# Performance work log

Measured on AMD Instinct MI355X. Metric: run time of the kernel, lower is better.

The kernel has to match this reference:

```python
import jax, jax.numpy as jnp
import numpy as np

# Config (from TheoreticalConfig, scaled to production size)
B = 4096          # batch_size
S = 128           # seq_len (max_seq_len)
DIM_Q = 512
DIM_Z = 64
DIM_U = 512
HID_V = 512       # assumed net_V hidden width
T_OFF = 20        # T_offline
T_ON = 10         # T_online
DT = 0.1
STIFF = 0.1       # stiffness
CSTIFF = 0.1      # contact_stiffness
MIN_DIM = min(DIM_U, DIM_Q)  # == DIM_Q here


def setup_inputs() -> dict:
    key = jax.random.key(0)
    ks = jax.random.split(key, 10)
    f32 = jnp.float32
    return {
        "u_seq": jax.random.normal(ks[0], (B, S, DIM_U), f32),
        "q0_off": jax.random.normal(ks[1], (B, DIM_Q), f32) * 0.1,
        "p0_off": jax.random.normal(ks[2], (B, DIM_Q), f32) * 0.1,
        "q0_on": jax.random.normal(ks[3], (B, DIM_Q), f32) * 0.1,
        "p0_on": jax.random.normal(ks[4], (B, DIM_Q), f32) * 0.1,
        "z": jax.random.normal(ks[5], (1, DIM_Z), f32) * 0.1,
        "W1": jax.random.normal(ks[6], (DIM_Q + DIM_Z, HID_V), f32) / np.sqrt(DIM_Q + DIM_Z).astype(np.float32),
        "b1": jnp.zeros((HID_V,), f32),
        "W2": jax.random.normal(ks[7], (HID_V, 1), f32) / np.sqrt(HID_V).astype(np.float32),
        "b2": jnp.zeros((1,), f32),
    }


def _net_V(qz, W1, b1, W2, b2):
    # small MLP potential: [B, dim_q+dim_z] -> [B, 1]
    return jnp.tanh(qz @ W1 + b1) @ W2 + b2


def _compute_H(q, p, s, z, W1, b1, W2, b2):
    # H^c = K + V_quad + V_net + Phi, all [B, 1]
    K = 0.5 * jnp.sum(p * p, axis=-1, keepdims=True)
    V_quad = 0.5 * STIFF * jnp.sum(q * q, axis=-1, keepdims=True)
    V_net = _net_V(jnp.concatenate([q, z], axis=-1), W1, b1, W2, b2)
    Phi = 0.5 * CSTIFF * s * s
    return K + V_quad + V_net + Phi


def reference(u_seq, q0_off, p0_off, q0_on, p0_on, z, W1, b1, W2, b2):
    zb = jnp.broadcast_to(z, (B, DIM_Z))
    s = jnp.zeros((B, 1), u_seq.dtype)

    # ---- evolve_offline: symplectic-ish leapfrog with friction, T_OFF-1 steps ----
    F0_off = _compute_H(q0_off, p0_off, s, zb, W1, b1, W2, b2)

    def off_step(carry, _):
        q, p = carry
        q_new = q + DT * p                     # q += dt * grad_p (grad_p = p)
        p_new = (p - DT * (STIFF * q)) * 0.99  # p -= dt * grad_q (grad_q = stiff*q_old), then damping
        return (q_new, p_new), None

    (qf, pf), _ = jax.lax.scan(off_step, (q0_off, p0_off), None, length=T_OFF - 1)
    Ff_off = _compute_H(qf, pf, s, zb, W1, b1, W2, b2)
    offline_F = jnp.concatenate([F0_off, Ff_off], axis=1)  # [B, 2]

    # ---- evolve_online: port-coupled integration for min(S, T_ON) steps ----
    F0_on = _compute_H(q0_on, p0_on, s, zb, W1, b1, W2, b2)
    steps = min(S, T_ON)

    def on_step(carry, u_t):
        q, p = carry
        # p_new[:, :MIN_DIM] = p - dt*stiff*q + dt*0.1*u_t ; MIN_DIM == DIM_Q so full update
        p_new = (p - DT * (STIFF * q) + DT * (0.1 * u_t)) * 0.99
        q_new = q + DT * p_new
        return (q_new, p_new), None

    u_scan = jnp.transpose(u_seq[:, :steps, :MIN_DIM], (1, 0, 2))  # [steps, B, dim_q]
    (qf2, pf2), _ = jax.lax.scan(on_step, (q0_on, p0_on), u_scan)
    Ff_on = _compute_H(qf2, pf2, s, zb, W1, b1, W2, b2)
    online_F = jnp.concatenate([F0_on, Ff_on], axis=1)  # [B, 2]

    q_trajectory = qf2[:, None, :]  # [B, 1, dim_q]
    return offline_F, online_F, q_trajectory
```

## Files before the change

### kernel.cpp

```cpp
#include <hip/hip_runtime.h>
#include <hip/hip_bf16.h>

#define BB 4096
#define SS 128
#define DIMQ 512
#define DIMZ 64
#define HIDV 512

typedef __attribute__((ext_vector_type(8))) short sh8;
typedef __attribute__((ext_vector_type(4))) float f32x4;
typedef __attribute__((ext_vector_type(4))) unsigned short us4;

__device__ inline unsigned short f2bf(float f) {
    unsigned u = __float_as_uint(f);
    return (unsigned short)((u + 0x7fffu + ((u >> 16) & 1u)) >> 16);
}

__global__ __launch_bounds__(256) void k_states_prep(
        const float* __restrict__ u, const float* __restrict__ q0off,
        const float* __restrict__ p0off, const float* __restrict__ q0on,
        const float* __restrict__ p0on, const float* __restrict__ b2,
        const float* __restrict__ W1, const float* __restrict__ z,
        const float* __restrict__ b1,
        unsigned short* __restrict__ Qall, unsigned short* __restrict__ W1qT,
        float* __restrict__ cvec, float* __restrict__ out,
        float* __restrict__ qtraj,
        float R00, float R01, float R10, float R11) {
    if (blockIdx.x >= 2048) {
        int pbi = blockIdx.x - 2048;
        __shared__ float tile[32][33];
        int bx = pbi & 15, by = pbi >> 4;
        int k0 = by * 32, n0 = bx * 32;
        int tx = threadIdx.x & 31, tg = threadIdx.x >> 5;
        #pragma unroll
        for (int rr = 0; rr < 4; rr++) {
            int ty = tg * 4 + rr;
            tile[ty][tx] = W1[(size_t)(k0 + ty) * HIDV + n0 + tx];
        }
        __syncthreads();
        #pragma unroll
        for (int rr = 0; rr < 4; rr++) {
            int ty = tg * 4 + rr;
            W1qT[(size_t)(n0 + ty) * DIMQ + k0 + tx] = f2bf(tile[tx][ty]);
        }
        if (pbi < 2) {
            int h = pbi * 256 + threadIdx.x;
            float acc = b1[h];
            #pragma unroll 8
            for (int k = 0; k < DIMZ; k++) acc += z[k] * W1[(size_t)(DIMQ + k) * HIDV + h];
            cvec[h] = acc;
        }
        return;
    }
    int t = threadIdx.x;
    int half = t >> 7;
    int tc = t & 127;
    int b = blockIdx.x * 2 + half;
    int j = tc * 4;
    size_t idx = (size_t)b * DIMQ + j;
    float q[4], p[4], qo[4], po[4];
    *(float4*)q  = *(const float4*)(q0off + idx);
    *(float4*)p  = *(const float4*)(p0off + idx);
    *(float4*)qo = *(const float4*)(q0on + idx);
    *(float4*)po = *(const float4*)(p0on + idx);

    float sums[8] = {0, 0, 0, 0, 0, 0, 0, 0};
    us4 w0, w1, w2, w3;
    float q2[4], p2[4];
    #pragma unroll
    for (int c = 0; c < 4; c++) {
        float qq = q[c], pp = p[c];
        sums[0] += qq * qq;
        sums[1] += pp * pp;
        float qf = R00 * qq + R01 * pp;
        float pf = R10 * qq + R11 * pp;
        sums[2] += qf * qf;
        sums[3] += pf * pf;
        w0[c] = f2bf(qq);
        w1[c] = f2bf(qf);
        q2[c] = qo[c]; p2[c] = po[c];
        sums[4] += q2[c] * q2[c];
        sums[5] += p2[c] * p2[c];
        w2[c] = f2bf(q2[c]);
    }
    *(us4*)(Qall + idx) = w0;
    *(us4*)(Qall + (size_t)(BB + b) * DIMQ + j) = w1;
    *(us4*)(Qall + (size_t)(2 * BB + b) * DIMQ + j) = w2;

    const float* ub = u + (size_t)b * SS * DIMQ + j;
    #pragma unroll
    for (int st = 0; st < 10; st++) {
        float uv[4];
        *(float4*)uv = *(const float4*)(ub + (size_t)st * DIMQ);
        #pragma unroll
        for (int c = 0; c < 4; c++) {
            p2[c] = (p2[c] - 0.1f * (0.1f * q2[c]) + 0.1f * (0.1f * uv[c])) * 0.99f;
            q2[c] = q2[c] + 0.1f * p2[c];
        }
    }
    #pragma unroll
    for (int c = 0; c < 4; c++) {
        sums[6] += q2[c] * q2[c];
        sums[7] += p2[c] * p2[c];
        w3[c] = f2bf(q2[c]);
    }
    *(us4*)(Qall + (size_t)(3 * BB + b) * DIMQ + j) = w3;
    *(float4*)(qtraj + idx) = *(float4*)q2;

    __shared__ float red[2][2][8];
    int lane = t & 63, wv = (t >> 6) & 1;
    #pragma unroll
    for (int k = 0; k < 8; k++) {
        float v = sums[k];
        #pragma unroll
        for (int m = 1; m < 64; m <<= 1) v += __shfl_xor(v, m, 64);
        if (lane == 0) red[half][wv][k] = v;
    }
    __syncthreads();
    if (tc < 4) {
        int e = tc;
        float sq = red[half][0][2 * e] + red[half][1][2 * e];
        float sp = red[half][0][2 * e + 1] + red[half][1][2 * e + 1];
        float F = 0.5f * sp + 0.05f * sq + b2[0];
        size_t o = (size_t)b * 2 + (e & 1) + (size_t)(e >> 1) * 2 * BB;
        out[o] = F;
    }
}

__global__ __launch_bounds__(256) void k_gemm(
        const unsigned short* __restrict__ Qall, const unsigned short* __restrict__ W1qT,
        const float* __restrict__ cvec, const float* __restrict__ W2,
        float* __restrict__ out) {
    __shared__ __attribute__((aligned(16))) char lds[65536];
    const int t = threadIdx.x;
    const int lane = t & 63;
    const int w = t >> 6;
    const int wr = w >> 1, wc = w & 1;
    const int rowBase = blockIdx.x * 128;
    const int colBase = blockIdx.y * 128;

    f32x4 acc[4][4] = {};

    auto STAGE = [&](int kt, int buf) {
        char* ldsA = lds + buf * 32768;
        char* ldsB = ldsA + 16384;
        #pragma unroll
        for (int i = 0; i < 4; i++) {
            unsigned chunk = i * 256 + t;
            unsigned r = chunk >> 3;
            unsigned scb = (chunk & 7) ^ (r & 7);
            const unsigned short* srcA = Qall + (size_t)(rowBase + r) * 512 + (unsigned)kt * 64 + scb * 8;
            __builtin_amdgcn_global_load_lds(
                (const __attribute__((address_space(1))) unsigned int*)(const void*)srcA,
                (__attribute__((address_space(3))) unsigned int*)(void*)(ldsA + chunk * 16), 16, 0, 0);
            const unsigned short* srcB = W1qT + (size_t)(colBase + r) * 512 + (unsigned)kt * 64 + scb * 8;
            __builtin_amdgcn_global_load_lds(
                (const __attribute__((address_space(1))) unsigned int*)(const void*)srcB,
                (__attribute__((address_space(3))) unsigned int*)(void*)(ldsB + chunk * 16), 16, 0, 0);
        }
    };

    STAGE(0, 0);
    asm volatile("s_waitcnt vmcnt(0)" ::: "memory");
    __builtin_amdgcn_s_barrier();

    for (int kt = 0; kt < 8; kt++) {
        int cur = kt & 1;
        if (kt < 7) STAGE(kt + 1, cur ^ 1);
        char* ldsA = lds + cur * 32768;
        char* ldsB = ldsA + 16384;
        #pragma unroll
        for (int ks = 0; ks < 2; ks++) {
            sh8 af[4], bf_[4];
            int kb = ks * 64 + ((lane >> 4) << 4);
            #pragma unroll
            for (int mi = 0; mi < 4; mi++) {
                int m = wr * 64 + mi * 16 + (lane & 15);
                af[mi] = *(const sh8*)(ldsA + m * 128 + (kb ^ ((m & 7) << 4)));
            }
            #pragma unroll
            for (int ni = 0; ni < 4; ni++) {
                int n = wc * 64 + ni * 16 + (lane & 15);
                bf_[ni] = *(const sh8*)(ldsB + n * 128 + (kb ^ ((n & 7) << 4)));
            }
            #pragma unroll
            for (int mi = 0; mi < 4; mi++)
                #pragma unroll
                for (int ni = 0; ni < 4; ni++)
                    acc[mi][ni] = __builtin_amdgcn_mfma_f32_16x16x32_bf16(af[mi], bf_[ni], acc[mi][ni], 0, 0, 0);
        }
        asm volatile("s_waitcnt vmcnt(0) lgkmcnt(0)" ::: "memory");
        __builtin_amdgcn_s_barrier();
    }

    float w2v[4], cv[4];
    #pragma unroll
    for (int ni = 0; ni < 4; ni++) {
        int n = colBase + wc * 64 + ni * 16 + (lane & 15);
        w2v[ni] = W2[n];
        cv[ni] = cvec[n];
    }
    #pragma unroll
    for (int mi = 0; mi < 4; mi++) {
        #pragma unroll
        for (int r = 0; r < 4; r++) {
            float partial = 0.f;
            #pragma unroll
            for (int ni = 0; ni < 4; ni++)
                partial += tanhf(acc[mi][ni][r] + cv[ni]) * w2v[ni];
            partial += __shfl_xor(partial, 1, 64);
            partial += __shfl_xor(partial, 2, 64);
            partial += __shfl_xor(partial, 4, 64);
            partial += __shfl_xor(partial, 8, 64);
            if ((lane & 15) == 0) {
                int row = rowBase + wr * 64 + mi * 16 + ((lane >> 4) << 2) + r;
                int e = row >> 12, bb = row & 4095;
                size_t o = (size_t)bb * 2 + (e & 1) + (size_t)(e >> 1) * 2 * BB;
                atomicAdd(out + o, partial);
            }
        }
    }
}

extern "C" void kernel_launch(void* const* d_in, const int* in_sizes, int n_in,
                              void* d_out, int out_size, void* d_ws, size_t ws_size,
                              hipStream_t stream) {
    const float* u     = (const float*)d_in[0];
    const float* q0off = (const float*)d_in[1];
    const float* p0off = (const float*)d_in[2];
    const float* q0on  = (const float*)d_in[3];
    const float* p0on  = (const float*)d_in[4];
    const float* z     = (const float*)d_in[5];
    const float* W1    = (const float*)d_in[6];
    const float* b1    = (const float*)d_in[7];
    const float* W2    = (const float*)d_in[8];
    const float* b2    = (const float*)d_in[9];
    float* out = (float*)d_out;

    char* ws = (char*)d_ws;
    unsigned short* Qall = (unsigned short*)ws;
    unsigned short* W1qT = (unsigned short*)(ws + 16777216);
    float* cvec = (float*)(ws + 16777216 + 524288);

    double a00 = 1, a01 = 0, a10 = 0, a11 = 1;
    const double m00 = 1.0, m01 = 0.1, m10 = -0.1 * 0.1 * 0.99, m11 = 0.99;
    for (int i = 0; i < 19; i++) {
        double n00 = m00 * a00 + m01 * a10;
        double n01 = m00 * a01 + m01 * a11;
        double n10 = m10 * a00 + m11 * a10;
        double n11 = m10 * a01 + m11 * a11;
        a00 = n00; a01 = n01; a10 = n10; a11 = n11;
    }

    k_states_prep<<<2304, 256, 0, stream>>>(u, q0off, p0off, q0on, p0on, b2,
                                            W1, z, b1, Qall, W1qT, cvec, out,
                                            out + 4 * BB,
                                            (float)a00, (float)a01, (float)a10, (float)a11);
    k_gemm<<<dim3(128, 4), 256, 0, stream>>>(Qall, W1qT, cvec, W2, out);
}
```

Before: 43.26 us.

## Fuse bf16 conversion into GEMM A-loads and overlap GEMM with state integration

Removes the intermediate bf16 Qall buffer. The GEMM now reads the fp32 q states directly, applying the offline rotation and converting to bf16 on the fly into LDS. Three of the four GEMM row-groups run inside the same kernel as the online integration, so the two can overlap, while a tail kernel handles the final-state GEMM from qtraj and folds in the accumulated Vnet values. This trades the 16MB workspace round trip for three launches, register-staged A loads that need more VGPRs, and larger fp32 A reads.

Measured after the change: 67.79 us. 56.7% more time.

```diff
diff --git a/kernel.cpp b/kernel.cpp
--- a/kernel.cpp
+++ b/kernel.cpp
@@ -9,53 +9,183 @@
 
 typedef __attribute__((ext_vector_type(8))) short sh8;
 typedef __attribute__((ext_vector_type(4))) float f32x4;
-typedef __attribute__((ext_vector_type(4))) unsigned short us4;
 
 __device__ inline unsigned short f2bf(float f) {
     unsigned u = __float_as_uint(f);
     return (unsigned short)((u + 0x7fffu + ((u >> 16) & 1u)) >> 16);
 }
 
-__global__ __launch_bounds__(256) void k_states_prep(
+__global__ __launch_bounds__(256) void k_prep(const float* __restrict__ W1,
+        const float* __restrict__ z, const float* __restrict__ b1,
+        unsigned short* __restrict__ W1qT, float* __restrict__ cvec,
+        float* __restrict__ Vnet) {
+    __shared__ float tile[32][33];
+    int bx = blockIdx.x & 15, by = blockIdx.x >> 4;
+    int k0 = by * 32, n0 = bx * 32;
+    int tx = threadIdx.x & 31, tg = threadIdx.x >> 5;
+    #pragma unroll
+    for (int rr = 0; rr < 4; rr++) {
+        int ty = tg * 4 + rr;
+        tile[ty][tx] = W1[(size_t)(k0 + ty) * HIDV + n0 + tx];
+    }
+    __syncthreads();
+    #pragma unroll
+    for (int rr = 0; rr < 4; rr++) {
+        int ty = tg * 4 + rr;
+        W1qT[(size_t)(n0 + ty) * DIMQ + k0 + tx] = f2bf(tile[tx][ty]);
+    }
+    if (blockIdx.x < 2) {
+        int h = blockIdx.x * 256 + threadIdx.x;
+        float acc = b1[h];
+        #pragma unroll 8
+        for (int k = 0; k < DIMZ; k++) acc += z[k] * W1[(size_t)(DIMQ + k) * HIDV + h];
+        cvec[h] = acc;
+    }
+    if (blockIdx.x < 12) {
+        int i = blockIdx.x * 1024 + threadIdx.x * 4;
+        float4 zv = {0.f, 0.f, 0.f, 0.f};
+        *(float4*)(Vnet + i) = zv;
+    }
+}
+
+__global__ __launch_bounds__(256) void k_main(
         const float* __restrict__ u, const float* __restrict__ q0off,
         const float* __restrict__ p0off, const float* __restrict__ q0on,
         const float* __restrict__ p0on, const float* __restrict__ b2,
-        const float* __restrict__ W1, const float* __restrict__ z,
-        const float* __restrict__ b1,
-        unsigned short* __restrict__ Qall, unsigned short* __restrict__ W1qT,
-        float* __restrict__ cvec, float* __restrict__ out,
-        float* __restrict__ qtraj,
+        const unsigned short* __restrict__ W1qT, const float* __restrict__ cvec,
+        const float* __restrict__ W2, float* __restrict__ Vnet,
+        float* __restrict__ out, float* __restrict__ qtraj,
         float R00, float R01, float R10, float R11) {
-    if (blockIdx.x >= 2048) {
-        int pbi = blockIdx.x - 2048;
-        __shared__ float tile[32][33];
-        int bx = pbi & 15, by = pbi >> 4;
-        int k0 = by * 32, n0 = bx * 32;
-        int tx = threadIdx.x & 31, tg = threadIdx.x >> 5;
-        #pragma unroll
-        for (int rr = 0; rr < 4; rr++) {
-            int ty = tg * 4 + rr;
-            tile[ty][tx] = W1[(size_t)(k0 + ty) * HIDV + n0 + tx];
-        }
-        __syncthreads();
-        #pragma unroll
-        for (int rr = 0; rr < 4; rr++) {
-            int ty = tg * 4 + rr;
-            W1qT[(size_t)(n0 + ty) * DIMQ + k0 + tx] = f2bf(tile[tx][ty]);
-        }
-        if (pbi < 2) {
-            int h = pbi * 256 + threadIdx.x;
-            float acc = b1[h];
-            #pragma unroll 8
-            for (int k = 0; k < DIMZ; k++) acc += z[k] * W1[(size_t)(DIMQ + k) * HIDV + h];
-            cvec[h] = acc;
+    __shared__ __attribute__((aligned(16))) char lds[65536];
+    const int t = threadIdx.x;
+
+    if (blockIdx.x < 384) {
+        const int gi = blockIdx.x;
+        const int e = gi >> 7;
+        const int rtc = gi & 127;
+        const int rowBase = (rtc >> 2) * 128;
+        const int colBase = (rtc & 3) * 128;
+        const int lane = t & 63;
+        const int w = t >> 6;
+        const int wr = w >> 1, wc = w & 1;
+        const float* srcA = (e == 2) ? q0on : q0off;
+
+        f32x4 acc[4][4] = {};
+        float4 Aq[4][2], Ap[4][2];
+
+        auto LOAD_A = [&](int kt) {
+            #pragma unroll
+            for (int i = 0; i < 4; i++) {
+                int ch = i * 256 + t, r = ch >> 3, cb = ch & 7;
+                const float* ba = srcA + (size_t)(rowBase + r) * 512 + kt * 64 + cb * 8;
+                Aq[i][0] = *(const float4*)ba;
+                Aq[i][1] = *(const float4*)(ba + 4);
+                if (e == 1) {
+                    const float* bp = p0off + (size_t)(rowBase + r) * 512 + kt * 64 + cb * 8;
+                    Ap[i][0] = *(const float4*)bp;
+                    Ap[i][1] = *(const float4*)(bp + 4);
+                }
+            }
+        };
+        auto WRITE_A = [&](int buf) {
+            char* dA = lds + buf * 16384;
+            #pragma unroll
+            for (int i = 0; i < 4; i++) {
+                int ch = i * 256 + t, r = ch >> 3, cb = ch & 7;
+                sh8 v;
+                #pragma unroll
+                for (int c2 = 0; c2 < 8; c2++) {
+                    float qv = (c2 < 4) ? Aq[i][0][c2] : Aq[i][1][c2 - 4];
+                    if (e == 1) {
+                        float pv = (c2 < 4) ? Ap[i][0][c2] : Ap[i][1][c2 - 4];
+                        qv = R00 * qv + R01 * pv;
+                    }
+                    v[c2] = (short)f2bf(qv);
+                }
+                *(sh8*)(dA + r * 128 + ((cb << 4) ^ ((r & 7) << 4))) = v;
+            }
+        };
+        auto STAGE_B = [&](int kt, int buf) {
+            char* dB = lds + 32768 + buf * 16384;
+            #pragma unroll
+            for (int i = 0; i < 4; i++) {
+                unsigned ch = i * 256 + t;
+                unsigned r = ch >> 3;
+                unsigned scb = (ch & 7) ^ (r & 7);
+                const unsigned short* src = W1qT + (size_t)(colBase + r) * 512 + (unsigned)kt * 64 + scb * 8;
+                __builtin_amdgcn_global_load_lds(
+                    (const __attribute__((address_space(1))) unsigned int*)(const void*)src,
+                    (__attribute__((address_space(3))) unsigned int*)(void*)(dB + ch * 16), 16, 0, 0);
+            }
+        };
+
+        LOAD_A(0);
+        STAGE_B(0, 0);
+        WRITE_A(0);
+        asm volatile("s_waitcnt vmcnt(0) lgkmcnt(0)" ::: "memory");
+        __builtin_amdgcn_s_barrier();
+
+        for (int kt = 0; kt < 8; kt++) {
+            int cur = kt & 1;
+            if (kt < 7) { LOAD_A(kt + 1); STAGE_B(kt + 1, cur ^ 1); }
+            char* ldsA = lds + cur * 16384;
+            char* ldsB = lds + 32768 + cur * 16384;
+            #pragma unroll
+            for (int ks = 0; ks < 2; ks++) {
+                sh8 af[4], bf_[4];
+                int kb = ks * 64 + ((lane >> 4) << 4);
+                #pragma unroll
+                for (int mi = 0; mi < 4; mi++) {
+                    int m = wr * 64 + mi * 16 + (lane & 15);
+                    af[mi] = *(const sh8*)(ldsA + m * 128 + (kb ^ ((m & 7) << 4)));
+                }
+                #pragma unroll
+                for (int ni = 0; ni < 4; ni++) {
+                    int n = wc * 64 + ni * 16 + (lane & 15);
+                    bf_[ni] = *(const sh8*)(ldsB + n * 128 + (kb ^ ((n & 7) << 4)));
+                }
+                #pragma unroll
+                for (int mi = 0; mi < 4; mi++)
+                    #pragma unroll
+                    for (int ni = 0; ni < 4; ni++)
+                        acc[mi][ni] = __builtin_amdgcn_mfma_f32_16x16x32_bf16(af[mi], bf_[ni], acc[mi][ni], 0, 0, 0);
+            }
+            if (kt < 7) WRITE_A(cur ^ 1);
+            asm volatile("s_waitcnt vmcnt(0) lgkmcnt(0)" ::: "memory");
+            __builtin_amdgcn_s_barrier();
+        }
+
+        float w2v[4], cv[4];
+        #pragma unroll
+        for (int ni = 0; ni < 4; ni++) {
+            int n = colBase + wc * 64 + ni * 16 + (lane & 15);
+            w2v[ni] = W2[n];
+            cv[ni] = cvec[n];
+        }
+        #pragma unroll
+        for (int mi = 0; mi < 4; mi++) {
+            #pragma unroll
+            for (int r = 0; r < 4; r++) {
+                float partial = 0.f;
+                #pragma unroll
+                for (int ni = 0; ni < 4; ni++)
+                    partial += tanhf(acc[mi][ni][r] + cv[ni]) * w2v[ni];
+                partial += __shfl_xor(partial, 1, 64);
+                partial += __shfl_xor(partial, 2, 64);
+                partial += __shfl_xor(partial, 4, 64);
+                partial += __shfl_xor(partial, 8, 64);
+                if ((lane & 15) == 0) {
+                    int row = rowBase + wr * 64 + mi * 16 + ((lane >> 4) << 2) + r;
+                    atomicAdd(Vnet + e * BB + row, partial);
+                }
+            }
         }
         return;
     }
-    int t = threadIdx.x;
+
     int half = t >> 7;
     int tc = t & 127;
-    int b = blockIdx.x * 2 + half;
+    int b = (blockIdx.x - 384) * 2 + half;
     int j = tc * 4;
     size_t idx = (size_t)b * DIMQ + j;
     float q[4], p[4], qo[4], po[4];
@@ -65,7 +195,6 @@
     *(float4*)po = *(const float4*)(p0on + idx);
 
     float sums[8] = {0, 0, 0, 0, 0, 0, 0, 0};
-    us4 w0, w1, w2, w3;
     float q2[4], p2[4];
     #pragma unroll
     for (int c = 0; c < 4; c++) {
@@ -76,17 +205,10 @@
         float pf = R10 * qq + R11 * pp;
         sums[2] += qf * qf;
         sums[3] += pf * pf;
-        w0[c] = f2bf(qq);
-        w1[c] = f2bf(qf);
         q2[c] = qo[c]; p2[c] = po[c];
         sums[4] += q2[c] * q2[c];
         sums[5] += p2[c] * p2[c];
-        w2[c] = f2bf(q2[c]);
-    }
-    *(us4*)(Qall + idx) = w0;
-    *(us4*)(Qall + (size_t)(BB + b) * DIMQ + j) = w1;
-    *(us4*)(Qall + (size_t)(2 * BB + b) * DIMQ + j) = w2;
-
+    }
     const float* ub = u + (size_t)b * SS * DIMQ + j;
     #pragma unroll
     for (int st = 0; st < 10; st++) {
@@ -102,73 +224,102 @@
     for (int c = 0; c < 4; c++) {
         sums[6] += q2[c] * q2[c];
         sums[7] += p2[c] * p2[c];
-        w3[c] = f2bf(q2[c]);
-    }
-    *(us4*)(Qall + (size_t)(3 * BB + b) * DIMQ + j) = w3;
+    }
     *(float4*)(qtraj + idx) = *(float4*)q2;
 
-    __shared__ float red[2][2][8];
+    float* red = (float*)lds;
     int lane = t & 63, wv = (t >> 6) & 1;
     #pragma unroll
     for (int k = 0; k < 8; k++) {
         float v = sums[k];
         #pragma unroll
         for (int m = 1; m < 64; m <<= 1) v += __shfl_xor(v, m, 64);
-        if (lane == 0) red[half][wv][k] = v;
+        if (lane == 0) red[(half * 2 + wv) * 8 + k] = v;
     }
     __syncthreads();
     if (tc < 4) {
         int e = tc;
-        float sq = red[half][0][2 * e] + red[half][1][2 * e];
-        float sp = red[half][0][2 * e + 1] + red[half][1][2 * e + 1];
+        float sq = red[(half * 2) * 8 + 2 * e] + red[(half * 2 + 1) * 8 + 2 * e];
+        float sp = red[(half * 2) * 8 + 2 * e + 1] + red[(half * 2 + 1) * 8 + 2 * e + 1];
         float F = 0.5f * sp + 0.05f * sq + b2[0];
         size_t o = (size_t)b * 2 + (e & 1) + (size_t)(e >> 1) * 2 * BB;
         out[o] = F;
     }
 }
 
-__global__ __launch_bounds__(256) void k_gemm(
-        const unsigned short* __restrict__ Qall, const unsigned short* __restrict__ W1qT,
+__global__ __launch_bounds__(256) void k_tail(
+        const float* __restrict__ qtraj, const unsigned short* __restrict__ W1qT,
         const float* __restrict__ cvec, const float* __restrict__ W2,
-        float* __restrict__ out) {
+        const float* __restrict__ Vnet, float* __restrict__ out) {
     __shared__ __attribute__((aligned(16))) char lds[65536];
     const int t = threadIdx.x;
+
+    if (blockIdx.x >= 128) {
+        int i = (blockIdx.x - 128) * 256 + t;
+        int e = i >> 12, b = i & 4095;
+        size_t o = (size_t)b * 2 + (e & 1) + (size_t)(e >> 1) * 2 * BB;
+        out[o] += Vnet[i];
+        return;
+    }
+
+    const int gi = blockIdx.x;
+    const int rowBase = (gi >> 2) * 128;
+    const int colBase = (gi & 3) * 128;
     const int lane = t & 63;
     const int w = t >> 6;
     const int wr = w >> 1, wc = w & 1;
-    const int rowBase = blockIdx.x * 128;
-    const int colBase = blockIdx.y * 128;
 
     f32x4 acc[4][4] = {};
-
-    auto STAGE = [&](int kt, int buf) {
-        char* ldsA = lds + buf * 32768;
-        char* ldsB = ldsA + 16384;
+    float4 Aq[4][2];
+
+    auto LOAD_A = [&](int kt) {
         #pragma unroll
         for (int i = 0; i < 4; i++) {
-            unsigned chunk = i * 256 + t;
-            unsigned r = chunk >> 3;
-            unsigned scb = (chunk & 7) ^ (r & 7);
-            const unsigned short* srcA = Qall + (size_t)(rowBase + r) * 512 + (unsigned)kt * 64 + scb * 8;
+            int ch = i * 256 + t, r = ch >> 3, cb = ch & 7;
+            const float* ba = qtraj + (size_t)(rowBase + r) * 512 + kt * 64 + cb * 8;
+            Aq[i][0] = *(const float4*)ba;
+            Aq[i][1] = *(const float4*)(ba + 4);
+        }
+    };
+    auto WRITE_A = [&](int buf) {
+        char* dA = lds + buf * 16384;
+        #pragma unroll
+        for (int i = 0; i < 4; i++) {
+            int ch = i * 256 + t, r = ch >> 3, cb = ch & 7;
+            sh8 v;
+            #pragma unroll
+            for (int c2 = 0; c2 < 8; c2++) {
+                float qv = (c2 < 4) ? Aq[i][0][c2] : Aq[i][1][c2 - 4];
+                v[c2] = (short)f2bf(qv);
+            }
+            *(sh8*)(dA + r * 128 + ((cb << 4) ^ ((r & 7) << 4))) = v;
+        }
+    };
+    auto STAGE_B = [&](int kt, int buf) {
+        char* dB = lds + 32768 + buf * 16384;
+        #pragma unroll
+        for (int i = 0; i < 4; i++) {
+            unsigned ch = i * 256 + t;
+            unsigned r = ch >> 3;
+            unsigned scb = (ch & 7) ^ (r & 7);
+            const unsigned short* src = W1qT + (size_t)(colBase + r) * 512 + (unsigned)kt * 64 + scb * 8;
             __builtin_amdgcn_global_load_lds(
-                (const __attribute__((address_space(1))) unsigned int*)(const void*)srcA,
-                (__attribute__((address_space(3))) unsigned int*)(void*)(ldsA + chunk * 16), 16, 0, 0);
-            const unsigned short* srcB = W1qT + (size_t)(colBase + r) * 512 + (unsigned)kt * 64 + scb * 8;
-            __builtin_amdgcn_global_load_lds(
-                (const __attribute__((address_space(1))) unsigned int*)(const void*)srcB,
-                (__attribute__((address_space(3))) unsigned int*)(void*)(ldsB + chunk * 16), 16, 0, 0);
+                (const __attribute__((address_space(1))) unsigned int*)(const void*)src,
+                (__attribute__((address_space(3))) unsigned int*)(void*)(dB + ch * 16), 16, 0, 0);
         }
     };
 
-    STAGE(0, 0);
-    asm volatile("s_waitcnt vmcnt(0)" ::: "memory");
+    LOAD_A(0);
+    STAGE_B(0, 0);
+    WRITE_A(0);
+    asm volatile("s_waitcnt vmcnt(0) lgkmcnt(0)" ::: "memory");
     __builtin_amdgcn_s_barrier();
 
     for (int kt = 0; kt < 8; kt++) {
         int cur = kt & 1;
-        if (kt < 7) STAGE(kt + 1, cur ^ 1);
-        char* ldsA = lds + cur * 32768;
-        char* ldsB = ldsA + 16384;
+        if (kt < 7) { LOAD_A(kt + 1); STAGE_B(kt + 1, cur ^ 1); }
+        char* ldsA = lds + cur * 16384;
+        char* ldsB = lds + 32768 + cur * 16384;
         #pragma unroll
         for (int ks = 0; ks < 2; ks++) {
             sh8 af[4], bf_[4];
@@ -189,6 +340,7 @@
                 for (int ni = 0; ni < 4; ni++)
                     acc[mi][ni] = __builtin_amdgcn_mfma_f32_16x16x32_bf16(af[mi], bf_[ni], acc[mi][ni], 0, 0, 0);
         }
+        if (kt < 7) WRITE_A(cur ^ 1);
         asm volatile("s_waitcnt vmcnt(0) lgkmcnt(0)" ::: "memory");
         __builtin_amdgcn_s_barrier();
     }
@@ -213,10 +365,8 @@
             partial += __shfl_xor(partial, 4, 64);
             partial += __shfl_xor(partial, 8, 64);
             if ((lane & 15) == 0) {
-                int row = rowBase + wr * 64 + mi * 16 + ((lane >> 4) << 2) + r;
-                int e = row >> 12, bb = row & 4095;
-                size_t o = (size_t)bb * 2 + (e & 1) + (size_t)(e >> 1) * 2 * BB;
-                atomicAdd(out + o, partial);
+                int b = rowBase + wr * 64 + mi * 16 + ((lane >> 4) << 2) + r;
+                atomicAdd(out + 2 * BB + (size_t)b * 2 + 1, partial);
             }
         }
     }
@@ -236,11 +386,12 @@
     const float* W2    = (const float*)d_in[8];
     const float* b2    = (const float*)d_in[9];
     float* out = (float*)d_out;
+    float* qtraj = out + 4 * BB;
 
     char* ws = (char*)d_ws;
-    unsigned short* Qall = (unsigned short*)ws;
-    unsigned short* W1qT = (unsigned short*)(ws + 16777216);
-    float* cvec = (float*)(ws + 16777216 + 524288);
+    unsigned short* W1qT = (unsigned short*)ws;
+    float* cvec = (float*)(ws + 524288);
+    float* Vnet = (float*)(ws + 524288 + 2048);
 
     double a00 = 1, a01 = 0, a10 = 0, a11 = 1;
     const double m00 = 1.0, m01 = 0.1, m10 = -0.1 * 0.1 * 0.99, m11 = 0.99;
@@ -252,9 +403,9 @@
         a00 = n00; a01 = n01; a10 = n10; a11 = n11;
     }
 
-    k_states_prep<<<2304, 256, 0, stream>>>(u, q0off, p0off, q0on, p0on, b2,
-                                            W1, z, b1, Qall, W1qT, cvec, out,
-                                            out + 4 * BB,
-                                            (float)a00, (float)a01, (float)a10, (float)a11);
-    k_gemm<<<dim3(128, 4), 256, 0, stream>>>(Qall, W1qT, cvec, W2, out);
+    k_prep<<<256, 256, 0, stream>>>(W1, z, b1, W1qT, cvec, Vnet);
+    k_main<<<2432, 256, 0, stream>>>(u, q0off, p0off, q0on, p0on, b2,
+                                     W1qT, cvec, W2, Vnet, out, qtraj,
+                                     (float)a00, (float)a01, (float)a10, (float)a11);
+    k_tail<<<176, 256, 0, stream>>>(qtraj, W1qT, cvec, W2, Vnet, out);
 }
```

## Fuse GEMM for input states into the elementwise kernel, reading fp32 directly

Applied to the files above, without the earlier changes.

Drops the bf16 staging buffer Qall. The three GEMM slices that depend only on inputs (initial offline, propagated offline, initial online) now run as extra blocks interleaved inside the elementwise kernel. Those blocks load fp32 rows straight from global memory, apply the 2x2 propagation matrix and convert to bf16 in registers. The final-online slice runs in a tail kernel that reads qtraj and also adds the accumulated Vnet into the output. This removes the 16 MB bf16 write and re-read and overlaps GEMM with the u-streaming work, but the GEMM gives up LDS staging and double buffering and uses smaller 64x128 tiles. It also adds a third kernel launch.

New measurement: 140.0 us. 3.24x slower.

```diff
diff --git a/kernel.cpp b/kernel.cpp
--- a/kernel.cpp
+++ b/kernel.cpp
@@ -9,53 +9,143 @@
 
 typedef __attribute__((ext_vector_type(8))) short sh8;
 typedef __attribute__((ext_vector_type(4))) float f32x4;
-typedef __attribute__((ext_vector_type(4))) unsigned short us4;
 
 __device__ inline unsigned short f2bf(float f) {
     unsigned u = __float_as_uint(f);
     return (unsigned short)((u + 0x7fffu + ((u >> 16) & 1u)) >> 16);
 }
 
-__global__ __launch_bounds__(256) void k_states_prep(
+__device__ __forceinline__ void gemm_tile(
+        int gi, bool isE1, const float* __restrict__ A0, const float* __restrict__ A1,
+        float R00, float R01,
+        const unsigned short* __restrict__ W1qT, const float* __restrict__ cvec,
+        const float* __restrict__ W2, float* __restrict__ tgt, int tgtMode, int t) {
+    const int lane = t & 63;
+    const int w = t >> 6;
+    const int rowBase = (gi >> 2) * 64 + (w >> 1) * 32;
+    const int colBase = (gi & 3) * 128 + (w & 1) * 64;
+    const int rr = lane & 15, g = lane >> 4;
+
+    f32x4 acc[2][4] = {};
+    for (int kt = 0; kt < 16; kt++) {
+        sh8 af[2];
+        #pragma unroll
+        for (int mi = 0; mi < 2; mi++) {
+            const float* pa = A0 + (size_t)(rowBase + mi * 16 + rr) * 512 + kt * 32 + g * 8;
+            float4 x0 = *(const float4*)pa;
+            float4 x1 = *(const float4*)(pa + 4);
+            if (isE1) {
+                const float* pb = A1 + (size_t)(rowBase + mi * 16 + rr) * 512 + kt * 32 + g * 8;
+                float4 y0 = *(const float4*)pb;
+                float4 y1 = *(const float4*)(pb + 4);
+                #pragma unroll
+                for (int j = 0; j < 4; j++) {
+                    x0[j] = R00 * x0[j] + R01 * y0[j];
+                    x1[j] = R00 * x1[j] + R01 * y1[j];
+                }
+            }
+            sh8 v;
+            #pragma unroll
+            for (int j = 0; j < 4; j++) {
+                v[j] = (short)f2bf(x0[j]);
+                v[4 + j] = (short)f2bf(x1[j]);
+            }
+            af[mi] = v;
+        }
+        sh8 bf_[4];
+        #pragma unroll
+        for (int ni = 0; ni < 4; ni++)
+            bf_[ni] = *(const sh8*)(W1qT + (size_t)(colBase + ni * 16 + rr) * 512 + kt * 32 + g * 8);
+        #pragma unroll
+        for (int mi = 0; mi < 2; mi++)
+            #pragma unroll
+            for (int ni = 0; ni < 4; ni++)
+                acc[mi][ni] = __builtin_amdgcn_mfma_f32_16x16x32_bf16(af[mi], bf_[ni], acc[mi][ni], 0, 0, 0);
+    }
+    float w2v[4], cv[4];
+    #pragma unroll
+    for (int ni = 0; ni < 4; ni++) {
+        int n = colBase + ni * 16 + rr;
+        w2v[ni] = W2[n];
+        cv[ni] = cvec[n];
+    }
+    #pragma unroll
+    for (int mi = 0; mi < 2; mi++) {
+        #pragma unroll
+        for (int r = 0; r < 4; r++) {
+            float s = 0.f;
+            #pragma unroll
+            for (int ni = 0; ni < 4; ni++)
+                s += tanhf(acc[mi][ni][r] + cv[ni]) * w2v[ni];
+            s += __shfl_xor(s, 1, 64);
+            s += __shfl_xor(s, 2, 64);
+            s += __shfl_xor(s, 4, 64);
+            s += __shfl_xor(s, 8, 64);
+            if (rr == 0) {
+                int row = rowBase + mi * 16 + g * 4 + r;
+                if (tgtMode == 0) atomicAdd(tgt + row, s);
+                else atomicAdd(tgt + (size_t)row * 2, s);
+            }
+        }
+    }
+}
+
+__global__ __launch_bounds__(256) void k_prep(const float* __restrict__ W1,
+        const float* __restrict__ z, const float* __restrict__ b1,
+        unsigned short* __restrict__ W1qT, float* __restrict__ cvec,
+        float* __restrict__ Vnet) {
+    __shared__ float tile[32][33];
+    int bx = blockIdx.x & 15, by = blockIdx.x >> 4;
+    int k0 = by * 32, n0 = bx * 32;
+    int tx = threadIdx.x & 31, tg = threadIdx.x >> 5;
+    #pragma unroll
+    for (int rr = 0; rr < 4; rr++) {
+        int ty = tg * 4 + rr;
+        tile[ty][tx] = W1[(size_t)(k0 + ty) * HIDV + n0 + tx];
+    }
+    __syncthreads();
+    #pragma unroll
+    for (int rr = 0; rr < 4; rr++) {
+        int ty = tg * 4 + rr;
+        W1qT[(size_t)(n0 + ty) * DIMQ + k0 + tx] = f2bf(tile[tx][ty]);
+    }
+    if (blockIdx.x < 2) {
+        int h = blockIdx.x * 256 + threadIdx.x;
+        float acc = b1[h];
+        #pragma unroll 8
+        for (int k = 0; k < DIMZ; k++) acc += z[k] * W1[(size_t)(DIMQ + k) * HIDV + h];
+        cvec[h] = acc;
+    }
+    if (blockIdx.x < 12) {
+        int i = blockIdx.x * 1024 + threadIdx.x * 4;
+        float4 zv = {0.f, 0.f, 0.f, 0.f};
+        *(float4*)(Vnet + i) = zv;
+    }
+}
+
+__global__ __launch_bounds__(256, 4) void k_main(
         const float* __restrict__ u, const float* __restrict__ q0off,
         const float* __restrict__ p0off, const float* __restrict__ q0on,
         const float* __restrict__ p0on, const float* __restrict__ b2,
-        const float* __restrict__ W1, const float* __restrict__ z,
-        const float* __restrict__ b1,
-        unsigned short* __restrict__ Qall, unsigned short* __restrict__ W1qT,
-        float* __restrict__ cvec, float* __restrict__ out,
-        float* __restrict__ qtraj,
+        const unsigned short* __restrict__ W1qT, const float* __restrict__ cvec,
+        const float* __restrict__ W2, float* __restrict__ Vnet,
+        float* __restrict__ out, float* __restrict__ qtraj,
         float R00, float R01, float R10, float R11) {
-    if (blockIdx.x >= 2048) {
-        int pbi = blockIdx.x - 2048;
-        __shared__ float tile[32][33];
-        int bx = pbi & 15, by = pbi >> 4;
-        int k0 = by * 32, n0 = bx * 32;
-        int tx = threadIdx.x & 31, tg = threadIdx.x >> 5;
-        #pragma unroll
-        for (int rr = 0; rr < 4; rr++) {
-            int ty = tg * 4 + rr;
-            tile[ty][tx] = W1[(size_t)(k0 + ty) * HIDV + n0 + tx];
-        }
-        __syncthreads();
-        #pragma unroll
-        for (int rr = 0; rr < 4; rr++) {
-            int ty = tg * 4 + rr;
-            W1qT[(size_t)(n0 + ty) * DIMQ + k0 + tx] = f2bf(tile[tx][ty]);
-        }
-        if (pbi < 2) {
-            int h = pbi * 256 + threadIdx.x;
-            float acc = b1[h];
-            #pragma unroll 8
-            for (int k = 0; k < DIMZ; k++) acc += z[k] * W1[(size_t)(DIMQ + k) * HIDV + h];
-            cvec[h] = acc;
-        }
+    const int t = threadIdx.x;
+    const int bid = blockIdx.x;
+    const int g1 = (int)(((long)bid * 768) / 2816);
+    const int g2 = (int)(((long)(bid + 1) * 768) / 2816);
+    if (g2 > g1) {
+        int e = g1 >> 8, gi = g1 & 255;
+        gemm_tile(gi, e == 1, (e == 2) ? q0on : q0off, p0off, R00, R01,
+                  W1qT, cvec, W2, Vnet + e * BB, 0, t);
         return;
     }
-    int t = threadIdx.x;
+
+    int sb = bid - g1;
     int half = t >> 7;
     int tc = t & 127;
-    int b = blockIdx.x * 2 + half;
+    int b = sb * 2 + half;
     int j = tc * 4;
     size_t idx = (size_t)b * DIMQ + j;
     float q[4], p[4], qo[4], po[4];
@@ -65,7 +155,6 @@
     *(float4*)po = *(const float4*)(p0on + idx);
 
     float sums[8] = {0, 0, 0, 0, 0, 0, 0, 0};
-    us4 w0, w1, w2, w3;
     float q2[4], p2[4];
     #pragma unroll
     for (int c = 0; c < 4; c++) {
@@ -76,17 +165,10 @@
         float pf = R10 * qq + R11 * pp;
         sums[2] += qf * qf;
         sums[3] += pf * pf;
-        w0[c] = f2bf(qq);
-        w1[c] = f2bf(qf);
         q2[c] = qo[c]; p2[c] = po[c];
         sums[4] += q2[c] * q2[c];
         sums[5] += p2[c] * p2[c];
-        w2[c] = f2bf(q2[c]);
-    }
-    *(us4*)(Qall + idx) = w0;
-    *(us4*)(Qall + (size_t)(BB + b) * DIMQ + j) = w1;
-    *(us4*)(Qall + (size_t)(2 * BB + b) * DIMQ + j) = w2;
-
+    }
     const float* ub = u + (size_t)b * SS * DIMQ + j;
     #pragma unroll
     for (int st = 0; st < 10; st++) {
@@ -102,124 +184,43 @@
     for (int c = 0; c < 4; c++) {
         sums[6] += q2[c] * q2[c];
         sums[7] += p2[c] * p2[c];
-        w3[c] = f2bf(q2[c]);
-    }
-    *(us4*)(Qall + (size_t)(3 * BB + b) * DIMQ + j) = w3;
+    }
     *(float4*)(qtraj + idx) = *(float4*)q2;
 
-    __shared__ float red[2][2][8];
+    __shared__ float red[32];
     int lane = t & 63, wv = (t >> 6) & 1;
     #pragma unroll
     for (int k = 0; k < 8; k++) {
         float v = sums[k];
         #pragma unroll
         for (int m = 1; m < 64; m <<= 1) v += __shfl_xor(v, m, 64);
-        if (lane == 0) red[half][wv][k] = v;
+        if (lane == 0) red[(half * 2 + wv) * 8 + k] = v;
     }
     __syncthreads();
     if (tc < 4) {
         int e = tc;
-        float sq = red[half][0][2 * e] + red[half][1][2 * e];
-        float sp = red[half][0][2 * e + 1] + red[half][1][2 * e + 1];
+        float sq = red[(half * 2) * 8 + 2 * e] + red[(half * 2 + 1) * 8 + 2 * e];
+        float sp = red[(half * 2) * 8 + 2 * e + 1] + red[(half * 2 + 1) * 8 + 2 * e + 1];
         float F = 0.5f * sp + 0.05f * sq + b2[0];
         size_t o = (size_t)b * 2 + (e & 1) + (size_t)(e >> 1) * 2 * BB;
         out[o] = F;
     }
 }
 
-__global__ __launch_bounds__(256) void k_gemm(
-        const unsigned short* __restrict__ Qall, const unsigned short* __restrict__ W1qT,
+__global__ __launch_bounds__(256) void k_tail(
+        const float* __restrict__ qtraj, const unsigned short* __restrict__ W1qT,
         const float* __restrict__ cvec, const float* __restrict__ W2,
-        float* __restrict__ out) {
-    __shared__ __attribute__((aligned(16))) char lds[65536];
+        const float* __restrict__ Vnet, float* __restrict__ out) {
     const int t = threadIdx.x;
-    const int lane = t & 63;
-    const int w = t >> 6;
-    const int wr = w >> 1, wc = w & 1;
-    const int rowBase = blockIdx.x * 128;
-    const int colBase = blockIdx.y * 128;
-
-    f32x4 acc[4][4] = {};
-
-    auto STAGE = [&](int kt, int buf) {
-        char* ldsA = lds + buf * 32768;
-        char* ldsB = ldsA + 16384;
-        #pragma unroll
-        for (int i = 0; i < 4; i++) {
-            unsigned chunk = i * 256 + t;
-            unsigned r = chunk >> 3;
-            unsigned scb = (chunk & 7) ^ (r & 7);
-            const unsigned short* srcA = Qall + (size_t)(rowBase + r) * 512 + (unsigned)kt * 64 + scb * 8;
-            __builtin_amdgcn_global_load_lds(
-                (const __attribute__((address_space(1))) unsigned int*)(const void*)srcA,
-                (__attribute__((address_space(3))) unsigned int*)(void*)(ldsA + chunk * 16), 16, 0, 0);
-            const unsigned short* srcB = W1qT + (size_t)(colBase + r) * 512 + (unsigned)kt * 64 + scb * 8;
-            __builtin_amdgcn_global_load_lds(
-                (const __attribute__((address_space(1))) unsigned int*)(const void*)srcB,
-                (__attribute__((address_space(3))) unsigned int*)(void*)(ldsB + chunk * 16), 16, 0, 0);
-        }
-    };
-
-    STAGE(0, 0);
-    asm volatile("s_waitcnt vmcnt(0)" ::: "memory");
-    __builtin_amdgcn_s_barrier();
-
-    for (int kt = 0; kt < 8; kt++) {
-        int cur = kt & 1;
-        if (kt < 7) STAGE(kt + 1, cur ^ 1);
-        char* ldsA = lds + cur * 32768;
-        char* ldsB = ldsA + 16384;
-        #pragma unroll
-        for (int ks = 0; ks < 2; ks++) {
-            sh8 af[4], bf_[4];
-            int kb = ks * 64 + ((lane >> 4) << 4);
-            #pragma unroll
-            for (int mi = 0; mi < 4; mi++) {
-                int m = wr * 64 + mi * 16 + (lane & 15);
-                af[mi] = *(const sh8*)(ldsA + m * 128 + (kb ^ ((m & 7) << 4)));
-            }
-            #pragma unroll
-            for (int ni = 0; ni < 4; ni++) {
-                int n = wc * 64 + ni * 16 + (lane & 15);
-                bf_[ni] = *(const sh8*)(ldsB + n * 128 + (kb ^ ((n & 7) << 4)));
-            }
-            #pragma unroll
-            for (int mi = 0; mi < 4; mi++)
-                #pragma unroll
-                for (int ni = 0; ni < 4; ni++)
-                    acc[mi][ni] = __builtin_amdgcn_mfma_f32_16x16x32_bf16(af[mi], bf_[ni], acc[mi][ni], 0, 0, 0);
-        }
-        asm volatile("s_waitcnt vmcnt(0) lgkmcnt(0)" ::: "memory");
-        __builtin_amdgcn_s_barrier();
-    }
-
-    float w2v[4], cv[4];
-    #pragma unroll
-    for (int ni = 0; ni < 4; ni++) {
-        int n = colBase + wc * 64 + ni * 16 + (lane & 15);
-        w2v[ni] = W2[n];
-        cv[ni] = cvec[n];
-    }
-    #pragma unroll
-    for (int mi = 0; mi < 4; mi++) {
-        #pragma unroll
-        for (int r = 0; r < 4; r++) {
-            float partial = 0.f;
-            #pragma unroll
-            for (int ni = 0; ni < 4; ni++)
-                partial += tanhf(acc[mi][ni][r] + cv[ni]) * w2v[ni];
-            partial += __shfl_xor(partial, 1, 64);
-            partial += __shfl_xor(partial, 2, 64);
-            partial += __shfl_xor(partial, 4, 64);
-            partial += __shfl_xor(partial, 8, 64);
-            if ((lane & 15) == 0) {
-                int row = rowBase + wr * 64 + mi * 16 + ((lane >> 4) << 2) + r;
-                int e = row >> 12, bb = row & 4095;
-                size_t o = (size_t)bb * 2 + (e & 1) + (size_t)(e >> 1) * 2 * BB;
-                atomicAdd(out + o, partial);
-            }
-        }
-    }
+    if (blockIdx.x >= 256) {
+        int i = (blockIdx.x - 256) * 256 + t;
+        int e = i >> 12, b = i & 4095;
+        size_t o = (size_t)b * 2 + (e & 1) + (size_t)(e >> 1) * 2 * BB;
+        out[o] += Vnet[i];
+        return;
+    }
+    gemm_tile(blockIdx.x, false, qtraj, nullptr, 0.f, 0.f,
+              W1qT, cvec, W2, out + 2 * BB + 1, 1, t);
 }
 
 extern "C" void kernel_launch(void* const* d_in, const int* in_sizes, int n_in,
@@ -236,11 +237,12 @@
     const float* W2    = (const float*)d_in[8];
     const float* b2    = (const float*)d_in[9];
     float* out = (float*)d_out;
+    float* qtraj = out + 4 * BB;
 
     char* ws = (char*)d_ws;
-    unsigned short* Qall = (unsigned short*)ws;
-    unsigned short* W1qT = (unsigned short*)(ws + 16777216);
-    float* cvec = (float*)(ws + 16777216 + 524288);
+    unsigned short* W1qT = (unsigned short*)ws;
+    float* cvec = (float*)(ws + 524288);
+    float* Vnet = (float*)(ws + 524288 + 2048);
 
     double a00 = 1, a01 = 0, a10 = 0, a11 = 1;
     const double m00 = 1.0, m01 = 0.1, m10 = -0.1 * 0.1 * 0.99, m11 = 0.99;
@@ -252,9 +254,9 @@
         a00 = n00; a01 = n01; a10 = n10; a11 = n11;
     }
 
-    k_states_prep<<<2304, 256, 0, stream>>>(u, q0off, p0off, q0on, p0on, b2,
-                                            W1, z, b1, Qall, W1qT, cvec, out,
-                                            out + 4 * BB,
-                                            (float)a00, (float)a01, (float)a10, (float)a11);
-    k_gemm<<<dim3(128, 4), 256, 0, stream>>>(Qall, W1qT, cvec, W2, out);
-}
+    k_prep<<<256, 256, 0, stream>>>(W1, z, b1, W1qT, cvec, Vnet);
+    k_main<<<2816, 256, 0, stream>>>(u, q0off, p0off, q0on, p0on, b2,
+                                     W1qT, cvec, W2, Vnet, out, qtraj,
+                                     (float)a00, (float)a01, (float)a10, (float)a11);
+    k_tail<<<304, 256, 0, stream>>>(qtraj, W1qT, cvec, W2, Vnet, out);
+}
```

## Use 8-wave blocks, triple-buffered LDS pipeline, and fast tanh in GEMM

Applied to the files above, without the earlier changes.

The GEMM kernel goes from 4 to 8 waves per block, each wave now computing a 64x32 tile, so there are more waves to hide latency. LDS staging becomes a three-buffer ring that prefetches two k-tiles ahead, with partial vmcnt waits replacing full drains, and uses 96KB of dynamic shared memory. tanhf is replaced by an exp/rcp approximation to make the epilogue cheaper. The larger LDS footprint can limit blocks per CU, and the fast tanh changes numerics slightly.

New measurement: 47.52 us. +9.8%, slower.

```diff
diff --git a/kernel.cpp b/kernel.cpp
--- a/kernel.cpp
+++ b/kernel.cpp
@@ -14,6 +14,11 @@
 __device__ inline unsigned short f2bf(float f) {
     unsigned u = __float_as_uint(f);
     return (unsigned short)((u + 0x7fffu + ((u >> 16) & 1u)) >> 16);
+}
+
+__device__ __forceinline__ float fast_tanh(float x) {
+    float e = __expf(2.0f * x);
+    return 1.0f - 2.0f * __builtin_amdgcn_rcpf(e + 1.0f);
 }
 
 __global__ __launch_bounds__(256) void k_states_prep(
@@ -127,26 +132,27 @@
     }
 }
 
-__global__ __launch_bounds__(256) void k_gemm(
+__global__ __launch_bounds__(512) void k_gemm(
         const unsigned short* __restrict__ Qall, const unsigned short* __restrict__ W1qT,
         const float* __restrict__ cvec, const float* __restrict__ W2,
         float* __restrict__ out) {
-    __shared__ __attribute__((aligned(16))) char lds[65536];
+    extern __shared__ char lds[];
     const int t = threadIdx.x;
     const int lane = t & 63;
+    const int g = lane >> 4, rr = lane & 15;
     const int w = t >> 6;
-    const int wr = w >> 1, wc = w & 1;
+    const int wr = w >> 2, wc = w & 3;
     const int rowBase = blockIdx.x * 128;
     const int colBase = blockIdx.y * 128;
 
-    f32x4 acc[4][4] = {};
+    f32x4 acc[4][2] = {};
 
     auto STAGE = [&](int kt, int buf) {
         char* ldsA = lds + buf * 32768;
         char* ldsB = ldsA + 16384;
         #pragma unroll
-        for (int i = 0; i < 4; i++) {
-            unsigned chunk = i * 256 + t;
+        for (int i = 0; i < 2; i++) {
+            unsigned chunk = i * 512 + t;
             unsigned r = chunk >> 3;
             unsigned scb = (chunk & 7) ^ (r & 7);
             const unsigned short* srcA = Qall + (size_t)(rowBase + r) * 512 + (unsigned)kt * 64 + scb * 8;
@@ -161,42 +167,49 @@
     };
 
     STAGE(0, 0);
-    asm volatile("s_waitcnt vmcnt(0)" ::: "memory");
+    STAGE(1, 1);
+    asm volatile("s_waitcnt vmcnt(4)" ::: "memory");
     __builtin_amdgcn_s_barrier();
 
     for (int kt = 0; kt < 8; kt++) {
-        int cur = kt & 1;
-        if (kt < 7) STAGE(kt + 1, cur ^ 1);
-        char* ldsA = lds + cur * 32768;
+        if (kt < 6) {
+            STAGE(kt + 2, (kt + 2) % 3);
+            asm volatile("s_waitcnt vmcnt(8)" ::: "memory");
+        } else if (kt == 6) {
+            asm volatile("s_waitcnt vmcnt(4)" ::: "memory");
+        } else {
+            asm volatile("s_waitcnt vmcnt(0)" ::: "memory");
+        }
+        char* ldsA = lds + (kt % 3) * 32768;
         char* ldsB = ldsA + 16384;
         #pragma unroll
         for (int ks = 0; ks < 2; ks++) {
-            sh8 af[4], bf_[4];
-            int kb = ks * 64 + ((lane >> 4) << 4);
+            sh8 af[4], bf_[2];
+            int kb = ks * 64 + (g << 4);
             #pragma unroll
             for (int mi = 0; mi < 4; mi++) {
-                int m = wr * 64 + mi * 16 + (lane & 15);
+                int m = wr * 64 + mi * 16 + rr;
                 af[mi] = *(const sh8*)(ldsA + m * 128 + (kb ^ ((m & 7) << 4)));
             }
             #pragma unroll
-            for (int ni = 0; ni < 4; ni++) {
-                int n = wc * 64 + ni * 16 + (lane & 15);
+            for (int ni = 0; ni < 2; ni++) {
+                int n = wc * 32 + ni * 16 + rr;
                 bf_[ni] = *(const sh8*)(ldsB + n * 128 + (kb ^ ((n & 7) << 4)));
             }
             #pragma unroll
             for (int mi = 0; mi < 4; mi++)
                 #pragma unroll
-                for (int ni = 0; ni < 4; ni++)
+                for (int ni = 0; ni < 2; ni++)
                     acc[mi][ni] = __builtin_amdgcn_mfma_f32_16x16x32_bf16(af[mi], bf_[ni], acc[mi][ni], 0, 0, 0);
         }
-        asm volatile("s_waitcnt vmcnt(0) lgkmcnt(0)" ::: "memory");
+        asm volatile("s_waitcnt lgkmcnt(0)" ::: "memory");
         __builtin_amdgcn_s_barrier();
     }
 
-    float w2v[4], cv[4];
-    #pragma unroll
-    for (int ni = 0; ni < 4; ni++) {
-        int n = colBase + wc * 64 + ni * 16 + (lane & 15);
+    float w2v[2], cv[2];
+    #pragma unroll
+    for (int ni = 0; ni < 2; ni++) {
+        int n = colBase + wc * 32 + ni * 16 + rr;
         w2v[ni] = W2[n];
         cv[ni] = cvec[n];
     }
@@ -206,14 +219,14 @@
         for (int r = 0; r < 4; r++) {
             float partial = 0.f;
             #pragma unroll
-            for (int ni = 0; ni < 4; ni++)
-                partial += tanhf(acc[mi][ni][r] + cv[ni]) * w2v[ni];
+            for (int ni = 0; ni < 2; ni++)
+                partial += fast_tanh(acc[mi][ni][r] + cv[ni]) * w2v[ni];
             partial += __shfl_xor(partial, 1, 64);
             partial += __shfl_xor(partial, 2, 64);
             partial += __shfl_xor(partial, 4, 64);
             partial += __shfl_xor(partial, 8, 64);
-            if ((lane & 15) == 0) {
-                int row = rowBase + wr * 64 + mi * 16 + ((lane >> 4) << 2) + r;
+            if (rr == 0) {
+                int row = rowBase + wr * 64 + mi * 16 + g * 4 + r;
                 int e = row >> 12, bb = row & 4095;
                 size_t o = (size_t)bb * 2 + (e & 1) + (size_t)(e >> 1) * 2 * BB;
                 atomicAdd(out + o, partial);
@@ -256,5 +269,5 @@
                                             W1, z, b1, Qall, W1qT, cvec, out,
                                             out + 4 * BB,
                                             (float)a00, (float)a01, (float)a10, (float)a11);
-    k_gemm<<<dim3(128, 4), 256, 0, stream>>>(Qall, W1qT, cvec, W2, out);
-}
+    k_gemm<<<dim3(128, 4), 512, 98304, stream>>>(Qall, W1qT, cvec, W2, out);
+}
```
